# Kernel optimization log

Hardware: AMD Instinct MI355X
Metric: run time of the kernel (lower is better)

The kernel has to match this reference:

```python
import jax, jax.numpy as jnp
import numpy as np


def setup_inputs() -> dict:
    key = jax.random.key(0)
    k1, k2 = jax.random.split(key)
    x = jax.random.normal(k1, (131072, 256), dtype=jnp.float32)
    centroids = jax.random.normal(k2, (2048, 256), dtype=jnp.float32)
    return {"x": x, "centroids": centroids}


def reference(x, centroids):
    """One k-means step: L2 nearest-centroid assignment + scatter-mean update.

    x:         (n, d) sample vectors
    centroids: (K, d) current centroids
    returns:   (K, d) new centroids
    """
    K = centroids.shape[0]
    # Squared L2 distance argmin; ||x||^2 term is constant per row, drop it.
    # scores[n, K] = ||c_k||^2 - 2 * x_n . c_k
    c_sq = jnp.sum(centroids * centroids, axis=-1)          # (K,)
    scores = c_sq[None, :] - 2.0 * jnp.einsum("nd,kd->nk", x, centroids)
    assigns = jnp.argmin(scores, axis=-1)                    # (n,) int
    # Segment mean update; keep old centroid for empty clusters.
    sums = jax.ops.segment_sum(x, assigns, num_segments=K)   # (K, d)
    counts = jax.ops.segment_sum(jnp.ones((x.shape[0],), x.dtype), assigns,
                                 num_segments=K)             # (K,)
    nonempty = counts > 0
    means = sums / jnp.maximum(counts, 1.0)[:, None]
    new_centroids = jnp.where(nonempty[:, None], means, centroids)
    return new_centroids
```

## Files before the change

### kernel.cpp

```cpp
#include <hip/hip_runtime.h>

typedef unsigned short u16;
typedef unsigned int u32;
typedef unsigned long long u64;
typedef __attribute__((ext_vector_type(4)))  int  i32x4;
typedef __attribute__((ext_vector_type(16))) int  i32x16;
typedef __attribute__((ext_vector_type(16))) char i8x16;

#define NPTS 131072
#define DIM  256
#define KC   2048

constexpr float S1  = 0.0625f;
constexpr float S2  = S1 / 254.0f;
constexpr float S3  = S2 * S2 / S1;
constexpr float IS1 = 16.0f;
constexpr float IS2 = 4064.0f;
constexpr float IS3 = 1.0f / S3;
constexpr float W_A = S1 * S1;
constexpr float R2  = 1.0f / 254.0f;

__device__ inline void quant3(float v, char& q1, char& q2, char& q3) {
    float a = fminf(fmaxf(rintf(v * IS1), -127.f), 127.f);
    float r1 = fmaf(-a, S1, v);
    float b = rintf(r1 * IS2);
    float r2 = fmaf(-b, S2, r1);
    float c = rintf(r2 * IS3);
    q1 = (char)a; q2 = (char)b; q3 = (char)c;
}

#define GLD16(gsrc, ldst) \
    __builtin_amdgcn_global_load_lds( \
        (const __attribute__((address_space(1))) void*)(gsrc), \
        (__attribute__((address_space(3))) void*)(ldst), 16, 0, 0)

__global__ void cprep_kernel(const float* __restrict__ cen,
                             char* __restrict__ c_q,
                             int* __restrict__ c_sqi,
                             int* __restrict__ hist) {
    if (blockIdx.x < 8) hist[blockIdx.x * 256 + threadIdx.x] = 0;
    const int lane = threadIdx.x & 63;
    const int wv   = threadIdx.x >> 6;
    const int n    = blockIdx.x * 4 + wv;
    float4 v = ((const float4*)(cen + (size_t)n * DIM))[lane];
    float ss = v.x * v.x + v.y * v.y + v.z * v.z + v.w * v.w;
    float fv[4] = {v.x, v.y, v.z, v.w};
    char q1[4], q2[4], q3[4];
#pragma unroll
    for (int j = 0; j < 4; ++j) quant3(fv[j], q1[j], q2[j], q3[j]);
    const int g = n >> 5, r32 = n & 31;
    const int s = lane >> 2;
    const size_t base = ((size_t)((g * 16 + s) * 32 + r32)) * 16 + (lane & 3) * 4;
    u32 p1 = (u32)(unsigned char)q1[0] | ((u32)(unsigned char)q1[1] << 8) |
             ((u32)(unsigned char)q1[2] << 16) | ((u32)(unsigned char)q1[3] << 24);
    u32 p2 = (u32)(unsigned char)q2[0] | ((u32)(unsigned char)q2[1] << 8) |
             ((u32)(unsigned char)q2[2] << 16) | ((u32)(unsigned char)q2[3] << 24);
    u32 p3 = (u32)(unsigned char)q3[0] | ((u32)(unsigned char)q3[1] << 8) |
             ((u32)(unsigned char)q3[2] << 16) | ((u32)(unsigned char)q3[3] << 24);
    *(u32*)(c_q + base) = p1;
    *(u32*)(c_q + (size_t)KC * DIM + base) = p2;
    *(u32*)(c_q + (size_t)2 * KC * DIM + base) = p3;
#pragma unroll
    for (int off = 32; off > 0; off >>= 1) ss += __shfl_xor(ss, off);
    if (lane == 0) c_sqi[n] = (int)rintf(ss * (0.5f * 254.0f / W_A));
}

__global__ __launch_bounds__(256, 3) void assign_kernel(
    const float* __restrict__ x, const char* __restrict__ c_q,
    const int* __restrict__ c_sqi, int* __restrict__ assigns,
    int* __restrict__ hist) {
    __shared__ char lds_c[3 * 12288 + 8192];

    const int tid  = threadIdx.x;
    const int lane = tid & 63;
    const int wv   = tid >> 6;
    const int l31  = lane & 31;
    const int kh   = lane >> 5;

    const char* cl1 = c_q;
    const char* cl2 = c_q + (size_t)KC * DIM;
    const char* cl3 = c_q + (size_t)2 * KC * DIM;

    GLD16((const char*)c_sqi + tid * 16,         lds_c + 36864 + tid * 16);
    GLD16((const char*)c_sqi + (tid + 256) * 16, lds_c + 36864 + (tid + 256) * 16);
    GLD16(cl1 + tid * 16,        lds_c + tid * 16);
    GLD16(cl2 + tid * 16,        lds_c + 4096 + tid * 16);
    GLD16(cl3 + tid * 16,        lds_c + 8192 + tid * 16);
    GLD16(cl1 + 4096 + tid * 16, lds_c + 12288 + tid * 16);
    GLD16(cl2 + 4096 + tid * 16, lds_c + 12288 + 4096 + tid * 16);
    GLD16(cl3 + 4096 + tid * 16, lds_c + 12288 + 8192 + tid * 16);

    const int m = blockIdx.x * 128 + wv * 32 + l31;
    const float4* xr = (const float4*)(x + (size_t)m * DIM);
    i8x16 xq1[8], xq2[8], xq3[8];
#pragma unroll
    for (int kt = 0; kt < 8; ++kt) {
        float tmp[16];
#pragma unroll
        for (int j = 0; j < 4; ++j) {
            float4 f = xr[kt * 8 + kh * 4 + j];
            tmp[j * 4 + 0] = f.x; tmp[j * 4 + 1] = f.y;
            tmp[j * 4 + 2] = f.z; tmp[j * 4 + 3] = f.w;
        }
        i8x16 v1, v2, v3;
#pragma unroll
        for (int j = 0; j < 16; ++j) {
            char a, b, c;
            quant3(tmp[j], a, b, c);
            v1[j] = a; v2[j] = b; v3[j] = c;
        }
        xq1[kt] = v1; xq2[kt] = v2; xq3[kt] = v3;
    }

    __syncthreads();

    float best = 3.4e38f;
    int bidx = 0;
    int b3 = 0;

    const int* csqL = (const int*)(lds_c + 36864);

    for (int t = 0; t < 64; ++t) {
        i32x16 accA = {}, accB = {}, accC = {};
#pragma unroll
        for (int h2 = 0; h2 < 2; ++h2) {
            if (t == 63 && h2 == 1) {
                asm volatile("s_waitcnt vmcnt(0)" ::: "memory");
            } else {
                asm volatile("s_waitcnt vmcnt(3)" ::: "memory");
            }
            __builtin_amdgcn_s_barrier();
            __builtin_amdgcn_sched_barrier(0);
            if (2 * t + h2 + 2 < 128) {
                int pn = b3 + 2; if (pn >= 3) pn -= 3;
                char* d = lds_c + pn * 12288;
                const size_t so = (size_t)(2 * t + h2 + 2) * 4096;
                GLD16(cl1 + so + tid * 16, d + tid * 16);
                GLD16(cl2 + so + tid * 16, d + 4096 + tid * 16);
                GLD16(cl3 + so + tid * 16, d + 8192 + tid * 16);
            }
            const char* cb = lds_c + b3 * 12288;
            __builtin_amdgcn_s_setprio(1);
#pragma unroll
            for (int kt2 = 0; kt2 < 4; ++kt2) {
                const int off = kt2 * 1024 + kh * 512 + l31 * 16;
                i32x4 c1 = __builtin_bit_cast(i32x4, *(const i8x16*)(cb + off));
                i32x4 c2 = __builtin_bit_cast(i32x4, *(const i8x16*)(cb + 4096 + off));
                i32x4 c3 = __builtin_bit_cast(i32x4, *(const i8x16*)(cb + 8192 + off));
                i32x4 x1 = __builtin_bit_cast(i32x4, xq1[h2 * 4 + kt2]);
                i32x4 x2 = __builtin_bit_cast(i32x4, xq2[h2 * 4 + kt2]);
                i32x4 x3 = __builtin_bit_cast(i32x4, xq3[h2 * 4 + kt2]);
                accA = __builtin_amdgcn_mfma_i32_32x32x32_i8(c1, x1, accA, 0, 0, 0);
                accB = __builtin_amdgcn_mfma_i32_32x32x32_i8(c1, x2, accB, 0, 0, 0);
                accC = __builtin_amdgcn_mfma_i32_32x32x32_i8(c2, x2, accC, 0, 0, 0);
                accB = __builtin_amdgcn_mfma_i32_32x32x32_i8(c2, x1, accB, 0, 0, 0);
                accC = __builtin_amdgcn_mfma_i32_32x32x32_i8(c1, x3, accC, 0, 0, 0);
                accC = __builtin_amdgcn_mfma_i32_32x32x32_i8(c3, x1, accC, 0, 0, 0);
            }
            __builtin_amdgcn_s_setprio(0);
            b3 += 1; if (b3 == 3) b3 = 0;
        }

#pragma unroll
        for (int bq = 0; bq < 4; ++bq) {
            int4 cs = *(const int4*)(csqL + (t * 8 + 2 * bq + kh) * 4);
            const int n0 = t * 32 + 8 * bq + 4 * kh;
            int csa[4] = {cs.x, cs.y, cs.z, cs.w};
#pragma unroll
            for (int r = 0; r < 4; ++r) {
                const int idx = bq * 4 + r;
                int D  = __mul24(accA[idx], 254) + accB[idx];
                int Vi = csa[r] - D;
                float v = fmaf((float)accC[idx], -R2, (float)Vi);
                if (v < best) { best = v; bidx = n0 + r; }
            }
        }
    }

    float oval = __shfl_xor(best, 32);
    int   oidx = __shfl_xor(bidx, 32);
    if (oval < best || (oval == best && oidx < bidx)) { best = oval; bidx = oidx; }
    if (lane < 32) {
        assigns[m] = bidx;
        atomicAdd(&hist[bidx], 1);
    }
}

__global__ void scan_kernel(const int* __restrict__ hist,
                            int* __restrict__ base_,
                            int* __restrict__ cursor) {
    __shared__ int tmp[256];
    const int tid = threadIdx.x;
    int v[8], s = 0;
#pragma unroll
    for (int j = 0; j < 8; ++j) { v[j] = hist[tid * 8 + j]; s += v[j]; }
    tmp[tid] = s;
    __syncthreads();
    for (int off = 1; off < 256; off <<= 1) {
        int t = (tid >= off) ? tmp[tid - off] : 0;
        __syncthreads();
        tmp[tid] += t;
        __syncthreads();
    }
    int ex = tmp[tid] - s;
#pragma unroll
    for (int j = 0; j < 8; ++j) {
        base_[tid * 8 + j] = ex;
        cursor[tid * 8 + j] = ex;
        ex += v[j];
    }
}

__global__ void reorder_kernel(const int* __restrict__ assigns,
                               int* __restrict__ cursor,
                               int* __restrict__ order) {
    const int p = blockIdx.x * 256 + threadIdx.x;
    const int a = assigns[p];
    int pos = atomicAdd(&cursor[a], 1);
    order[pos] = p;
}

__global__ void reduce_kernel(const float* __restrict__ x,
                              const int* __restrict__ order,
                              const int* __restrict__ assigns,
                              float* __restrict__ sums) {
    const int tid = threadIdx.x;
    const int r0 = blockIdx.x * 256;
    float acc = 0.f;
    int cur = assigns[order[r0]];
    for (int r = 0; r < 256; r += 4) {
        int p0 = order[r0 + r + 0], p1 = order[r0 + r + 1];
        int p2 = order[r0 + r + 2], p3 = order[r0 + r + 3];
        float v0 = x[(size_t)p0 * DIM + tid];
        float v1 = x[(size_t)p1 * DIM + tid];
        float v2 = x[(size_t)p2 * DIM + tid];
        float v3 = x[(size_t)p3 * DIM + tid];
        int a0 = assigns[p0], a1 = assigns[p1], a2 = assigns[p2], a3 = assigns[p3];
        if (a0 != cur) { unsafeAtomicAdd(&sums[(size_t)cur * DIM + tid], acc); acc = 0.f; cur = a0; }
        acc += v0;
        if (a1 != cur) { unsafeAtomicAdd(&sums[(size_t)cur * DIM + tid], acc); acc = 0.f; cur = a1; }
        acc += v1;
        if (a2 != cur) { unsafeAtomicAdd(&sums[(size_t)cur * DIM + tid], acc); acc = 0.f; cur = a2; }
        acc += v2;
        if (a3 != cur) { unsafeAtomicAdd(&sums[(size_t)cur * DIM + tid], acc); acc = 0.f; cur = a3; }
        acc += v3;
    }
    unsafeAtomicAdd(&sums[(size_t)cur * DIM + tid], acc);
}

__global__ void finalize_kernel(const float* __restrict__ sums,
                                const int* __restrict__ hist,
                                const float* __restrict__ cen,
                                float* __restrict__ out) {
    const int id = blockIdx.x * 256 + threadIdx.x;
    const int k = id >> 6;
    const int cnt = hist[k];
    float4 s = ((const float4*)sums)[id];
    float4 c = ((const float4*)cen)[id];
    float4 o;
    if (cnt > 0) {
        float r = 1.0f / (float)cnt;
        o.x = s.x * r; o.y = s.y * r; o.z = s.z * r; o.w = s.w * r;
    } else {
        o = c;
    }
    ((float4*)out)[id] = o;
}

extern "C" void kernel_launch(void* const* d_in, const int* in_sizes, int n_in,
                              void* d_out, int out_size, void* d_ws, size_t ws_size,
                              hipStream_t stream) {
    (void)in_sizes; (void)n_in; (void)out_size; (void)ws_size;
    const float* x   = (const float*)d_in[0];
    const float* cen = (const float*)d_in[1];
    float* out = (float*)d_out;

    char* ws = (char*)d_ws;
    size_t off = 0;
    char* c_q = (char*)(ws + off);           off += (size_t)3 * KC * DIM;
    int* c_sqi = (int*)(ws + off);           off += (size_t)KC * 4;
    int* assigns = (int*)(ws + off);         off += (size_t)NPTS * 4;
    int* hist = (int*)(ws + off);            off += (size_t)KC * 4;
    int* base_ = (int*)(ws + off);           off += (size_t)KC * 4;
    int* cursor = (int*)(ws + off);          off += (size_t)KC * 4;
    int* order = (int*)(ws + off);           off += (size_t)NPTS * 4;
    float* sums = (float*)(ws + off);        off += (size_t)KC * DIM * 4;

    hipMemsetAsync(sums, 0, (size_t)KC * DIM * sizeof(float), stream);
    cprep_kernel<<<KC / 4, 256, 0, stream>>>(cen, c_q, c_sqi, hist);
    assign_kernel<<<NPTS / 128, 256, 0, stream>>>(x, c_q, c_sqi, assigns, hist);
    scan_kernel<<<1, 256, 0, stream>>>(hist, base_, cursor);
    reorder_kernel<<<NPTS / 256, 256, 0, stream>>>(assigns, cursor, order);
    reduce_kernel<<<NPTS / 256, 256, 0, stream>>>(x, order, assigns, sums);
    finalize_kernel<<<KC * 64 / 256, 256, 0, stream>>>(sums, hist, cen, out);
}
```

Measured before the change: 615.3 us.

## Switch centroid staging to double buffering, split accumulator chain, fuse sums zeroing

The assign kernel's LDS staging goes from a triple-buffered ring with a vmcnt(3) lookahead to a double buffer that waits on vmcnt(0) before each barrier. This cuts LDS use from about 45 KB to about 33 KB per block, which could let more blocks share a CU. The accC dependency chain of three MFMAs is split into two accumulators (accC and accC2) that are summed at the end, which shortens the serial MFMA dependence. The separate hipMemsetAsync of sums is folded into cprep_kernel, dropping one launch; the cost is less prefetch lookahead, so load latency may be exposed more often.

```diff
diff --git a/kernel.cpp b/kernel.cpp
--- a/kernel.cpp
+++ b/kernel.cpp
@@ -37,8 +37,10 @@
 __global__ void cprep_kernel(const float* __restrict__ cen,
                              char* __restrict__ c_q,
                              int* __restrict__ c_sqi,
-                             int* __restrict__ hist) {
+                             int* __restrict__ hist,
+                             float* __restrict__ sums) {
     if (blockIdx.x < 8) hist[blockIdx.x * 256 + threadIdx.x] = 0;
+    ((float4*)sums)[blockIdx.x * 256 + threadIdx.x] = (float4){0.f, 0.f, 0.f, 0.f};
     const int lane = threadIdx.x & 63;
     const int wv   = threadIdx.x >> 6;
     const int n    = blockIdx.x * 4 + wv;
@@ -69,7 +71,7 @@
     const float* __restrict__ x, const char* __restrict__ c_q,
     const int* __restrict__ c_sqi, int* __restrict__ assigns,
     int* __restrict__ hist) {
-    __shared__ char lds_c[3 * 12288 + 8192];
+    __shared__ char lds_c[2 * 12288 + 8192];
 
     const int tid  = threadIdx.x;
     const int lane = tid & 63;
@@ -81,14 +83,11 @@
     const char* cl2 = c_q + (size_t)KC * DIM;
     const char* cl3 = c_q + (size_t)2 * KC * DIM;
 
-    GLD16((const char*)c_sqi + tid * 16,         lds_c + 36864 + tid * 16);
-    GLD16((const char*)c_sqi + (tid + 256) * 16, lds_c + 36864 + (tid + 256) * 16);
-    GLD16(cl1 + tid * 16,        lds_c + tid * 16);
-    GLD16(cl2 + tid * 16,        lds_c + 4096 + tid * 16);
-    GLD16(cl3 + tid * 16,        lds_c + 8192 + tid * 16);
-    GLD16(cl1 + 4096 + tid * 16, lds_c + 12288 + tid * 16);
-    GLD16(cl2 + 4096 + tid * 16, lds_c + 12288 + 4096 + tid * 16);
-    GLD16(cl3 + 4096 + tid * 16, lds_c + 12288 + 8192 + tid * 16);
+    GLD16((const char*)c_sqi + tid * 16,         lds_c + 24576 + tid * 16);
+    GLD16((const char*)c_sqi + (tid + 256) * 16, lds_c + 24576 + (tid + 256) * 16);
+    GLD16(cl1 + tid * 16, lds_c + tid * 16);
+    GLD16(cl2 + tid * 16, lds_c + 4096 + tid * 16);
+    GLD16(cl3 + tid * 16, lds_c + 8192 + tid * 16);
 
     const int m = blockIdx.x * 128 + wv * 32 + l31;
     const float4* xr = (const float4*)(x + (size_t)m * DIM);
@@ -112,34 +111,27 @@
         xq1[kt] = v1; xq2[kt] = v2; xq3[kt] = v3;
     }
 
-    __syncthreads();
-
     float best = 3.4e38f;
     int bidx = 0;
-    int b3 = 0;
-
-    const int* csqL = (const int*)(lds_c + 36864);
+
+    const int* csqL = (const int*)(lds_c + 24576);
 
     for (int t = 0; t < 64; ++t) {
-        i32x16 accA = {}, accB = {}, accC = {};
+        i32x16 accA = {}, accB = {}, accC = {}, accC2 = {};
 #pragma unroll
         for (int h2 = 0; h2 < 2; ++h2) {
-            if (t == 63 && h2 == 1) {
-                asm volatile("s_waitcnt vmcnt(0)" ::: "memory");
-            } else {
-                asm volatile("s_waitcnt vmcnt(3)" ::: "memory");
-            }
+            const int u = 2 * t + h2;
+            asm volatile("s_waitcnt vmcnt(0)" ::: "memory");
             __builtin_amdgcn_s_barrier();
             __builtin_amdgcn_sched_barrier(0);
-            if (2 * t + h2 + 2 < 128) {
-                int pn = b3 + 2; if (pn >= 3) pn -= 3;
-                char* d = lds_c + pn * 12288;
-                const size_t so = (size_t)(2 * t + h2 + 2) * 4096;
+            if (u + 1 < 128) {
+                char* d = lds_c + ((u + 1) & 1) * 12288;
+                const size_t so = (size_t)(u + 1) * 4096;
                 GLD16(cl1 + so + tid * 16, d + tid * 16);
                 GLD16(cl2 + so + tid * 16, d + 4096 + tid * 16);
                 GLD16(cl3 + so + tid * 16, d + 8192 + tid * 16);
             }
-            const char* cb = lds_c + b3 * 12288;
+            const char* cb = lds_c + (u & 1) * 12288;
             __builtin_amdgcn_s_setprio(1);
 #pragma unroll
             for (int kt2 = 0; kt2 < 4; ++kt2) {
@@ -150,15 +142,14 @@
                 i32x4 x1 = __builtin_bit_cast(i32x4, xq1[h2 * 4 + kt2]);
                 i32x4 x2 = __builtin_bit_cast(i32x4, xq2[h2 * 4 + kt2]);
                 i32x4 x3 = __builtin_bit_cast(i32x4, xq3[h2 * 4 + kt2]);
-                accA = __builtin_amdgcn_mfma_i32_32x32x32_i8(c1, x1, accA, 0, 0, 0);
-                accB = __builtin_amdgcn_mfma_i32_32x32x32_i8(c1, x2, accB, 0, 0, 0);
-                accC = __builtin_amdgcn_mfma_i32_32x32x32_i8(c2, x2, accC, 0, 0, 0);
-                accB = __builtin_amdgcn_mfma_i32_32x32x32_i8(c2, x1, accB, 0, 0, 0);
-                accC = __builtin_amdgcn_mfma_i32_32x32x32_i8(c1, x3, accC, 0, 0, 0);
-                accC = __builtin_amdgcn_mfma_i32_32x32x32_i8(c3, x1, accC, 0, 0, 0);
+                accA  = __builtin_amdgcn_mfma_i32_32x32x32_i8(c1, x1, accA,  0, 0, 0);
+                accB  = __builtin_amdgcn_mfma_i32_32x32x32_i8(c1, x2, accB,  0, 0, 0);
+                accC2 = __builtin_amdgcn_mfma_i32_32x32x32_i8(c1, x3, accC2, 0, 0, 0);
+                accC  = __builtin_amdgcn_mfma_i32_32x32x32_i8(c2, x2, accC,  0, 0, 0);
+                accB  = __builtin_amdgcn_mfma_i32_32x32x32_i8(c2, x1, accB,  0, 0, 0);
+                accC2 = __builtin_amdgcn_mfma_i32_32x32x32_i8(c3, x1, accC2, 0, 0, 0);
             }
             __builtin_amdgcn_s_setprio(0);
-            b3 += 1; if (b3 == 3) b3 = 0;
         }
 
 #pragma unroll
@@ -170,8 +161,9 @@
             for (int r = 0; r < 4; ++r) {
                 const int idx = bq * 4 + r;
                 int D  = __mul24(accA[idx], 254) + accB[idx];
+                int Ci = accC[idx] + accC2[idx];
                 int Vi = csa[r] - D;
-                float v = fmaf((float)accC[idx], -R2, (float)Vi);
+                float v = fmaf((float)Ci, -R2, (float)Vi);
                 if (v < best) { best = v; bidx = n0 + r; }
             }
         }
@@ -286,8 +278,7 @@
     int* order = (int*)(ws + off);           off += (size_t)NPTS * 4;
     float* sums = (float*)(ws + off);        off += (size_t)KC * DIM * 4;
 
-    hipMemsetAsync(sums, 0, (size_t)KC * DIM * sizeof(float), stream);
-    cprep_kernel<<<KC / 4, 256, 0, stream>>>(cen, c_q, c_sqi, hist);
+    cprep_kernel<<<KC / 4, 256, 0, stream>>>(cen, c_q, c_sqi, hist, sums);
     assign_kernel<<<NPTS / 128, 256, 0, stream>>>(x, c_q, c_sqi, assigns, hist);
     scan_kernel<<<1, 256, 0, stream>>>(hist, base_, cursor);
     reorder_kernel<<<NPTS / 256, 256, 0, stream>>>(assigns, cursor, order);
```

Result: slower. 678.8 us (+10.3%).

## Process two 32-row point tiles per wave and fold sums memset into cprep

Applied to the files above, without the earlier changes.

Each wave now quantizes and scores 64 points instead of 32, reusing every centroid fragment loaded from LDS across two sets of MFMA accumulators. This halves the LDS reads and centroid staging per point, and the block count drops by half. In exchange, register pressure roughly doubles, so launch bounds go from 3 to 2 blocks per CU. The separate memset of the sums buffer is removed, and cprep_kernel now zeroes it, which saves a launch. The __syncthreads after the x quantization was also dropped, but the loop's first waitcnt and barrier still cover the initial LDS loads.

```diff
diff --git a/kernel.cpp b/kernel.cpp
--- a/kernel.cpp
+++ b/kernel.cpp
@@ -29,6 +29,25 @@
     q1 = (char)a; q2 = (char)b; q3 = (char)c;
 }
 
+__device__ inline void quant_frag(const float4* __restrict__ xr, int kt, int kh,
+                                  i8x16& o1, i8x16& o2, i8x16& o3) {
+    float tmp[16];
+#pragma unroll
+    for (int j = 0; j < 4; ++j) {
+        float4 f = xr[kt * 8 + kh * 4 + j];
+        tmp[j * 4 + 0] = f.x; tmp[j * 4 + 1] = f.y;
+        tmp[j * 4 + 2] = f.z; tmp[j * 4 + 3] = f.w;
+    }
+    i8x16 v1, v2, v3;
+#pragma unroll
+    for (int j = 0; j < 16; ++j) {
+        char a, b, c;
+        quant3(tmp[j], a, b, c);
+        v1[j] = a; v2[j] = b; v3[j] = c;
+    }
+    o1 = v1; o2 = v2; o3 = v3;
+}
+
 #define GLD16(gsrc, ldst) \
     __builtin_amdgcn_global_load_lds( \
         (const __attribute__((address_space(1))) void*)(gsrc), \
@@ -37,8 +56,10 @@
 __global__ void cprep_kernel(const float* __restrict__ cen,
                              char* __restrict__ c_q,
                              int* __restrict__ c_sqi,
-                             int* __restrict__ hist) {
+                             int* __restrict__ hist,
+                             float* __restrict__ sums) {
     if (blockIdx.x < 8) hist[blockIdx.x * 256 + threadIdx.x] = 0;
+    ((float4*)sums)[blockIdx.x * 256 + threadIdx.x] = (float4){0.f, 0.f, 0.f, 0.f};
     const int lane = threadIdx.x & 63;
     const int wv   = threadIdx.x >> 6;
     const int n    = blockIdx.x * 4 + wv;
@@ -65,7 +86,7 @@
     if (lane == 0) c_sqi[n] = (int)rintf(ss * (0.5f * 254.0f / W_A));
 }
 
-__global__ __launch_bounds__(256, 3) void assign_kernel(
+__global__ __launch_bounds__(256, 2) void assign_kernel(
     const float* __restrict__ x, const char* __restrict__ c_q,
     const int* __restrict__ c_sqi, int* __restrict__ assigns,
     int* __restrict__ hist) {
@@ -90,38 +111,27 @@
     GLD16(cl2 + 4096 + tid * 16, lds_c + 12288 + 4096 + tid * 16);
     GLD16(cl3 + 4096 + tid * 16, lds_c + 12288 + 8192 + tid * 16);
 
-    const int m = blockIdx.x * 128 + wv * 32 + l31;
-    const float4* xr = (const float4*)(x + (size_t)m * DIM);
-    i8x16 xq1[8], xq2[8], xq3[8];
+    const int mbase = blockIdx.x * 256 + wv * 64;
+    const int mA = mbase + l31;
+    const int mB = mA + 32;
+    const float4* xrA = (const float4*)(x + (size_t)mA * DIM);
+    const float4* xrB = (const float4*)(x + (size_t)mB * DIM);
+    i8x16 xa1[8], xa2[8], xa3[8], xb1[8], xb2[8], xb3[8];
 #pragma unroll
     for (int kt = 0; kt < 8; ++kt) {
-        float tmp[16];
-#pragma unroll
-        for (int j = 0; j < 4; ++j) {
-            float4 f = xr[kt * 8 + kh * 4 + j];
-            tmp[j * 4 + 0] = f.x; tmp[j * 4 + 1] = f.y;
-            tmp[j * 4 + 2] = f.z; tmp[j * 4 + 3] = f.w;
-        }
-        i8x16 v1, v2, v3;
-#pragma unroll
-        for (int j = 0; j < 16; ++j) {
-            char a, b, c;
-            quant3(tmp[j], a, b, c);
-            v1[j] = a; v2[j] = b; v3[j] = c;
-        }
-        xq1[kt] = v1; xq2[kt] = v2; xq3[kt] = v3;
-    }
-
-    __syncthreads();
-
-    float best = 3.4e38f;
-    int bidx = 0;
+        quant_frag(xrA, kt, kh, xa1[kt], xa2[kt], xa3[kt]);
+        quant_frag(xrB, kt, kh, xb1[kt], xb2[kt], xb3[kt]);
+    }
+
+    float bestA = 3.4e38f, bestB = 3.4e38f;
+    int bixA = 0, bixB = 0;
     int b3 = 0;
 
     const int* csqL = (const int*)(lds_c + 36864);
 
     for (int t = 0; t < 64; ++t) {
-        i32x16 accA = {}, accB = {}, accC = {};
+        i32x16 accAa = {}, accBa = {}, accCa = {};
+        i32x16 accAb = {}, accBb = {}, accCb = {};
 #pragma unroll
         for (int h2 = 0; h2 < 2; ++h2) {
             if (t == 63 && h2 == 1) {
@@ -147,15 +157,25 @@
                 i32x4 c1 = __builtin_bit_cast(i32x4, *(const i8x16*)(cb + off));
                 i32x4 c2 = __builtin_bit_cast(i32x4, *(const i8x16*)(cb + 4096 + off));
                 i32x4 c3 = __builtin_bit_cast(i32x4, *(const i8x16*)(cb + 8192 + off));
-                i32x4 x1 = __builtin_bit_cast(i32x4, xq1[h2 * 4 + kt2]);
-                i32x4 x2 = __builtin_bit_cast(i32x4, xq2[h2 * 4 + kt2]);
-                i32x4 x3 = __builtin_bit_cast(i32x4, xq3[h2 * 4 + kt2]);
-                accA = __builtin_amdgcn_mfma_i32_32x32x32_i8(c1, x1, accA, 0, 0, 0);
-                accB = __builtin_amdgcn_mfma_i32_32x32x32_i8(c1, x2, accB, 0, 0, 0);
-                accC = __builtin_amdgcn_mfma_i32_32x32x32_i8(c2, x2, accC, 0, 0, 0);
-                accB = __builtin_amdgcn_mfma_i32_32x32x32_i8(c2, x1, accB, 0, 0, 0);
-                accC = __builtin_amdgcn_mfma_i32_32x32x32_i8(c1, x3, accC, 0, 0, 0);
-                accC = __builtin_amdgcn_mfma_i32_32x32x32_i8(c3, x1, accC, 0, 0, 0);
+                const int kq = h2 * 4 + kt2;
+                i32x4 a1 = __builtin_bit_cast(i32x4, xa1[kq]);
+                i32x4 a2 = __builtin_bit_cast(i32x4, xa2[kq]);
+                i32x4 a3 = __builtin_bit_cast(i32x4, xa3[kq]);
+                i32x4 b1 = __builtin_bit_cast(i32x4, xb1[kq]);
+                i32x4 b2 = __builtin_bit_cast(i32x4, xb2[kq]);
+                i32x4 b3v = __builtin_bit_cast(i32x4, xb3[kq]);
+                accAa = __builtin_amdgcn_mfma_i32_32x32x32_i8(c1, a1, accAa, 0, 0, 0);
+                accAb = __builtin_amdgcn_mfma_i32_32x32x32_i8(c1, b1, accAb, 0, 0, 0);
+                accBa = __builtin_amdgcn_mfma_i32_32x32x32_i8(c1, a2, accBa, 0, 0, 0);
+                accBb = __builtin_amdgcn_mfma_i32_32x32x32_i8(c1, b2, accBb, 0, 0, 0);
+                accCa = __builtin_amdgcn_mfma_i32_32x32x32_i8(c2, a2, accCa, 0, 0, 0);
+                accCb = __builtin_amdgcn_mfma_i32_32x32x32_i8(c2, b2, accCb, 0, 0, 0);
+                accBa = __builtin_amdgcn_mfma_i32_32x32x32_i8(c2, a1, accBa, 0, 0, 0);
+                accBb = __builtin_amdgcn_mfma_i32_32x32x32_i8(c2, b1, accBb, 0, 0, 0);
+                accCa = __builtin_amdgcn_mfma_i32_32x32x32_i8(c1, a3, accCa, 0, 0, 0);
+                accCb = __builtin_amdgcn_mfma_i32_32x32x32_i8(c1, b3v, accCb, 0, 0, 0);
+                accCa = __builtin_amdgcn_mfma_i32_32x32x32_i8(c3, a1, accCa, 0, 0, 0);
+                accCb = __builtin_amdgcn_mfma_i32_32x32x32_i8(c3, b1, accCb, 0, 0, 0);
             }
             __builtin_amdgcn_s_setprio(0);
             b3 += 1; if (b3 == 3) b3 = 0;
@@ -169,21 +189,25 @@
 #pragma unroll
             for (int r = 0; r < 4; ++r) {
                 const int idx = bq * 4 + r;
-                int D  = __mul24(accA[idx], 254) + accB[idx];
-                int Vi = csa[r] - D;
-                float v = fmaf((float)accC[idx], -R2, (float)Vi);
-                if (v < best) { best = v; bidx = n0 + r; }
+                int Da = __mul24(accAa[idx], 254) + accBa[idx];
+                float va = fmaf((float)accCa[idx], -R2, (float)(csa[r] - Da));
+                if (va < bestA) { bestA = va; bixA = n0 + r; }
+                int Db = __mul24(accAb[idx], 254) + accBb[idx];
+                float vb = fmaf((float)accCb[idx], -R2, (float)(csa[r] - Db));
+                if (vb < bestB) { bestB = vb; bixB = n0 + r; }
             }
         }
     }
 
-    float oval = __shfl_xor(best, 32);
-    int   oidx = __shfl_xor(bidx, 32);
-    if (oval < best || (oval == best && oidx < bidx)) { best = oval; bidx = oidx; }
-    if (lane < 32) {
-        assigns[m] = bidx;
-        atomicAdd(&hist[bidx], 1);
-    }
+    float ovA = __shfl_xor(bestA, 32);
+    int   oiA = __shfl_xor(bixA, 32);
+    if (ovA < bestA || (ovA == bestA && oiA < bixA)) { bestA = ovA; bixA = oiA; }
+    float ovB = __shfl_xor(bestB, 32);
+    int   oiB = __shfl_xor(bixB, 32);
+    if (ovB < bestB || (ovB == bestB && oiB < bixB)) { bestB = ovB; bixB = oiB; }
+    const int myIdx = (lane < 32) ? bixA : bixB;
+    assigns[mbase + lane] = myIdx;
+    atomicAdd(&hist[myIdx], 1);
 }
 
 __global__ void scan_kernel(const int* __restrict__ hist,
@@ -286,9 +310,8 @@
     int* order = (int*)(ws + off);           off += (size_t)NPTS * 4;
     float* sums = (float*)(ws + off);        off += (size_t)KC * DIM * 4;
 
-    hipMemsetAsync(sums, 0, (size_t)KC * DIM * sizeof(float), stream);
-    cprep_kernel<<<KC / 4, 256, 0, stream>>>(cen, c_q, c_sqi, hist);
-    assign_kernel<<<NPTS / 128, 256, 0, stream>>>(x, c_q, c_sqi, assigns, hist);
+    cprep_kernel<<<KC / 4, 256, 0, stream>>>(cen, c_q, c_sqi, hist, sums);
+    assign_kernel<<<NPTS / 256, 256, 0, stream>>>(x, c_q, c_sqi, assigns, hist);
     scan_kernel<<<1, 256, 0, stream>>>(hist, base_, cursor);
     reorder_kernel<<<NPTS / 256, 256, 0, stream>>>(assigns, cursor, order);
     reduce_kernel<<<NPTS / 256, 256, 0, stream>>>(x, order, assigns, sums);
```

New measurement: 749.2 us. 1.22x slower.

## Split centroid range into halves with persistent work-queue assign kernel and atomicMin merge

Applied to the files above, without the earlier changes.

The assign kernel becomes persistent with 768 blocks that pull work items from an atomic counter. Each item covers 128 points against half of the centroids, and partial argmins are merged through a 64-bit atomicMin on a packed (score, index) key. A new resolve kernel then writes the assignments and the histogram. Zeroing of sums moves from a memset into cprep, and the C accumulator is split in two to shorten the MFMA dependency chain. The aim is better load balance and fewer wave-quantization tail effects, at the cost of quantizing x twice per point, extra atomics and one extra kernel launch.

```diff
diff --git a/kernel.cpp b/kernel.cpp
--- a/kernel.cpp
+++ b/kernel.cpp
@@ -10,6 +10,7 @@
 #define NPTS 131072
 #define DIM  256
 #define KC   2048
+#define NITEMS 2048
 
 constexpr float S1  = 0.0625f;
 constexpr float S2  = S1 / 254.0f;
@@ -29,6 +30,25 @@
     q1 = (char)a; q2 = (char)b; q3 = (char)c;
 }
 
+__device__ inline void quant_frag(const float4* __restrict__ xr, int kt, int kh,
+                                  i8x16& o1, i8x16& o2, i8x16& o3) {
+    float tmp[16];
+#pragma unroll
+    for (int j = 0; j < 4; ++j) {
+        float4 f = xr[kt * 8 + kh * 4 + j];
+        tmp[j * 4 + 0] = f.x; tmp[j * 4 + 1] = f.y;
+        tmp[j * 4 + 2] = f.z; tmp[j * 4 + 3] = f.w;
+    }
+    i8x16 v1, v2, v3;
+#pragma unroll
+    for (int j = 0; j < 16; ++j) {
+        char a, b, c;
+        quant3(tmp[j], a, b, c);
+        v1[j] = a; v2[j] = b; v3[j] = c;
+    }
+    o1 = v1; o2 = v2; o3 = v3;
+}
+
 #define GLD16(gsrc, ldst) \
     __builtin_amdgcn_global_load_lds( \
         (const __attribute__((address_space(1))) void*)(gsrc), \
@@ -37,8 +57,14 @@
 __global__ void cprep_kernel(const float* __restrict__ cen,
                              char* __restrict__ c_q,
                              int* __restrict__ c_sqi,
-                             int* __restrict__ hist) {
+                             int* __restrict__ hist,
+                             float* __restrict__ sums,
+                             u64* __restrict__ best_key,
+                             int* __restrict__ work) {
     if (blockIdx.x < 8) hist[blockIdx.x * 256 + threadIdx.x] = 0;
+    if (blockIdx.x == 8 && threadIdx.x == 0) *work = 0;
+    ((float4*)sums)[blockIdx.x * 256 + threadIdx.x] = (float4){0.f, 0.f, 0.f, 0.f};
+    best_key[blockIdx.x * 256 + threadIdx.x] = ~0ull;
     const int lane = threadIdx.x & 63;
     const int wv   = threadIdx.x >> 6;
     const int n    = blockIdx.x * 4 + wv;
@@ -67,9 +93,10 @@
 
 __global__ __launch_bounds__(256, 3) void assign_kernel(
     const float* __restrict__ x, const char* __restrict__ c_q,
-    const int* __restrict__ c_sqi, int* __restrict__ assigns,
-    int* __restrict__ hist) {
+    const int* __restrict__ c_sqi, u64* __restrict__ best_key,
+    int* __restrict__ work) {
     __shared__ char lds_c[3 * 12288 + 8192];
+    __shared__ int item_s;
 
     const int tid  = threadIdx.x;
     const int lane = tid & 63;
@@ -77,113 +104,119 @@
     const int l31  = lane & 31;
     const int kh   = lane >> 5;
 
-    const char* cl1 = c_q;
-    const char* cl2 = c_q + (size_t)KC * DIM;
-    const char* cl3 = c_q + (size_t)2 * KC * DIM;
-
     GLD16((const char*)c_sqi + tid * 16,         lds_c + 36864 + tid * 16);
     GLD16((const char*)c_sqi + (tid + 256) * 16, lds_c + 36864 + (tid + 256) * 16);
-    GLD16(cl1 + tid * 16,        lds_c + tid * 16);
-    GLD16(cl2 + tid * 16,        lds_c + 4096 + tid * 16);
-    GLD16(cl3 + tid * 16,        lds_c + 8192 + tid * 16);
-    GLD16(cl1 + 4096 + tid * 16, lds_c + 12288 + tid * 16);
-    GLD16(cl2 + 4096 + tid * 16, lds_c + 12288 + 4096 + tid * 16);
-    GLD16(cl3 + 4096 + tid * 16, lds_c + 12288 + 8192 + tid * 16);
-
-    const int m = blockIdx.x * 128 + wv * 32 + l31;
-    const float4* xr = (const float4*)(x + (size_t)m * DIM);
-    i8x16 xq1[8], xq2[8], xq3[8];
-#pragma unroll
-    for (int kt = 0; kt < 8; ++kt) {
-        float tmp[16];
-#pragma unroll
-        for (int j = 0; j < 4; ++j) {
-            float4 f = xr[kt * 8 + kh * 4 + j];
-            tmp[j * 4 + 0] = f.x; tmp[j * 4 + 1] = f.y;
-            tmp[j * 4 + 2] = f.z; tmp[j * 4 + 3] = f.w;
-        }
-        i8x16 v1, v2, v3;
-#pragma unroll
-        for (int j = 0; j < 16; ++j) {
-            char a, b, c;
-            quant3(tmp[j], a, b, c);
-            v1[j] = a; v2[j] = b; v3[j] = c;
-        }
-        xq1[kt] = v1; xq2[kt] = v2; xq3[kt] = v3;
-    }
-
-    __syncthreads();
-
-    float best = 3.4e38f;
-    int bidx = 0;
-    int b3 = 0;
-
     const int* csqL = (const int*)(lds_c + 36864);
 
-    for (int t = 0; t < 64; ++t) {
-        i32x16 accA = {}, accB = {}, accC = {};
-#pragma unroll
-        for (int h2 = 0; h2 < 2; ++h2) {
-            if (t == 63 && h2 == 1) {
-                asm volatile("s_waitcnt vmcnt(0)" ::: "memory");
-            } else {
-                asm volatile("s_waitcnt vmcnt(3)" ::: "memory");
+    for (;;) {
+        if (tid == 0) item_s = atomicAdd(work, 1);
+        __syncthreads();
+        const int it = item_s;
+        if (it >= NITEMS) break;
+        const int pc = it >> 1;
+        const int h  = it & 1;
+
+        const char* cl1 = c_q + (size_t)h * 262144;
+        const char* cl2 = c_q + (size_t)KC * DIM + (size_t)h * 262144;
+        const char* cl3 = c_q + (size_t)2 * KC * DIM + (size_t)h * 262144;
+
+        GLD16(cl1 + tid * 16,        lds_c + tid * 16);
+        GLD16(cl2 + tid * 16,        lds_c + 4096 + tid * 16);
+        GLD16(cl3 + tid * 16,        lds_c + 8192 + tid * 16);
+        GLD16(cl1 + 4096 + tid * 16, lds_c + 12288 + tid * 16);
+        GLD16(cl2 + 4096 + tid * 16, lds_c + 12288 + 4096 + tid * 16);
+        GLD16(cl3 + 4096 + tid * 16, lds_c + 12288 + 8192 + tid * 16);
+
+        const int m = pc * 128 + wv * 32 + l31;
+        const float4* xr = (const float4*)(x + (size_t)m * DIM);
+        i8x16 xq1[8], xq2[8], xq3[8];
+#pragma unroll
+        for (int kt = 0; kt < 8; ++kt)
+            quant_frag(xr, kt, kh, xq1[kt], xq2[kt], xq3[kt]);
+
+        float best = 3.4e38f;
+        int bidx = 0;
+        int b3 = 0;
+
+        for (int t = 0; t < 32; ++t) {
+            i32x16 accA = {}, accB = {}, accC = {}, accC2 = {};
+#pragma unroll
+            for (int h2 = 0; h2 < 2; ++h2) {
+                const int u = 2 * t + h2;
+                if (u == 63) {
+                    asm volatile("s_waitcnt vmcnt(0)" ::: "memory");
+                } else {
+                    asm volatile("s_waitcnt vmcnt(3)" ::: "memory");
+                }
+                __builtin_amdgcn_s_barrier();
+                __builtin_amdgcn_sched_barrier(0);
+                if (u + 2 < 64) {
+                    int pn = b3 + 2; if (pn >= 3) pn -= 3;
+                    char* d = lds_c + pn * 12288;
+                    const size_t so = (size_t)(u + 2) * 4096;
+                    GLD16(cl1 + so + tid * 16, d + tid * 16);
+                    GLD16(cl2 + so + tid * 16, d + 4096 + tid * 16);
+                    GLD16(cl3 + so + tid * 16, d + 8192 + tid * 16);
+                }
+                const char* cb = lds_c + b3 * 12288;
+                __builtin_amdgcn_s_setprio(1);
+#pragma unroll
+                for (int kt2 = 0; kt2 < 4; ++kt2) {
+                    const int off = kt2 * 1024 + kh * 512 + l31 * 16;
+                    i32x4 c1 = __builtin_bit_cast(i32x4, *(const i8x16*)(cb + off));
+                    i32x4 c2 = __builtin_bit_cast(i32x4, *(const i8x16*)(cb + 4096 + off));
+                    i32x4 c3 = __builtin_bit_cast(i32x4, *(const i8x16*)(cb + 8192 + off));
+                    i32x4 x1 = __builtin_bit_cast(i32x4, xq1[h2 * 4 + kt2]);
+                    i32x4 x2 = __builtin_bit_cast(i32x4, xq2[h2 * 4 + kt2]);
+                    i32x4 x3 = __builtin_bit_cast(i32x4, xq3[h2 * 4 + kt2]);
+                    accA  = __builtin_amdgcn_mfma_i32_32x32x32_i8(c1, x1, accA,  0, 0, 0);
+                    accB  = __builtin_amdgcn_mfma_i32_32x32x32_i8(c1, x2, accB,  0, 0, 0);
+                    accC2 = __builtin_amdgcn_mfma_i32_32x32x32_i8(c1, x3, accC2, 0, 0, 0);
+                    accC  = __builtin_amdgcn_mfma_i32_32x32x32_i8(c2, x2, accC,  0, 0, 0);
+                    accB  = __builtin_amdgcn_mfma_i32_32x32x32_i8(c2, x1, accB,  0, 0, 0);
+                    accC2 = __builtin_amdgcn_mfma_i32_32x32x32_i8(c3, x1, accC2, 0, 0, 0);
+                }
+                __builtin_amdgcn_s_setprio(0);
+                b3 += 1; if (b3 == 3) b3 = 0;
             }
-            __builtin_amdgcn_s_barrier();
-            __builtin_amdgcn_sched_barrier(0);
-            if (2 * t + h2 + 2 < 128) {
-                int pn = b3 + 2; if (pn >= 3) pn -= 3;
-                char* d = lds_c + pn * 12288;
-                const size_t so = (size_t)(2 * t + h2 + 2) * 4096;
-                GLD16(cl1 + so + tid * 16, d + tid * 16);
-                GLD16(cl2 + so + tid * 16, d + 4096 + tid * 16);
-                GLD16(cl3 + so + tid * 16, d + 8192 + tid * 16);
-            }
-            const char* cb = lds_c + b3 * 12288;
-            __builtin_amdgcn_s_setprio(1);
-#pragma unroll
-            for (int kt2 = 0; kt2 < 4; ++kt2) {
-                const int off = kt2 * 1024 + kh * 512 + l31 * 16;
-                i32x4 c1 = __builtin_bit_cast(i32x4, *(const i8x16*)(cb + off));
-                i32x4 c2 = __builtin_bit_cast(i32x4, *(const i8x16*)(cb + 4096 + off));
-                i32x4 c3 = __builtin_bit_cast(i32x4, *(const i8x16*)(cb + 8192 + off));
-                i32x4 x1 = __builtin_bit_cast(i32x4, xq1[h2 * 4 + kt2]);
-                i32x4 x2 = __builtin_bit_cast(i32x4, xq2[h2 * 4 + kt2]);
-                i32x4 x3 = __builtin_bit_cast(i32x4, xq3[h2 * 4 + kt2]);
-                accA = __builtin_amdgcn_mfma_i32_32x32x32_i8(c1, x1, accA, 0, 0, 0);
-                accB = __builtin_amdgcn_mfma_i32_32x32x32_i8(c1, x2, accB, 0, 0, 0);
-                accC = __builtin_amdgcn_mfma_i32_32x32x32_i8(c2, x2, accC, 0, 0, 0);
-                accB = __builtin_amdgcn_mfma_i32_32x32x32_i8(c2, x1, accB, 0, 0, 0);
-                accC = __builtin_amdgcn_mfma_i32_32x32x32_i8(c1, x3, accC, 0, 0, 0);
-                accC = __builtin_amdgcn_mfma_i32_32x32x32_i8(c3, x1, accC, 0, 0, 0);
-            }
-            __builtin_amdgcn_s_setprio(0);
-            b3 += 1; if (b3 == 3) b3 = 0;
-        }
-
-#pragma unroll
-        for (int bq = 0; bq < 4; ++bq) {
-            int4 cs = *(const int4*)(csqL + (t * 8 + 2 * bq + kh) * 4);
-            const int n0 = t * 32 + 8 * bq + 4 * kh;
-            int csa[4] = {cs.x, cs.y, cs.z, cs.w};
-#pragma unroll
-            for (int r = 0; r < 4; ++r) {
-                const int idx = bq * 4 + r;
-                int D  = __mul24(accA[idx], 254) + accB[idx];
-                int Vi = csa[r] - D;
-                float v = fmaf((float)accC[idx], -R2, (float)Vi);
-                if (v < best) { best = v; bidx = n0 + r; }
+
+            const int nt = h * 32 + t;
+#pragma unroll
+            for (int bq = 0; bq < 4; ++bq) {
+                int4 cs = *(const int4*)(csqL + (nt * 8 + 2 * bq + kh) * 4);
+                const int n0 = nt * 32 + 8 * bq + 4 * kh;
+                int csa[4] = {cs.x, cs.y, cs.z, cs.w};
+#pragma unroll
+                for (int r = 0; r < 4; ++r) {
+                    const int idx = bq * 4 + r;
+                    int D  = __mul24(accA[idx], 254) + accB[idx];
+                    int Ci = accC[idx] + accC2[idx];
+                    int Vi = csa[r] - D;
+                    float v = fmaf((float)Ci, -R2, (float)Vi);
+                    if (v < best) { best = v; bidx = n0 + r; }
+                }
             }
         }
-    }
-
-    float oval = __shfl_xor(best, 32);
-    int   oidx = __shfl_xor(bidx, 32);
-    if (oval < best || (oval == best && oidx < bidx)) { best = oval; bidx = oidx; }
-    if (lane < 32) {
-        assigns[m] = bidx;
-        atomicAdd(&hist[bidx], 1);
-    }
+
+        float oval = __shfl_xor(best, 32);
+        int   oidx = __shfl_xor(bidx, 32);
+        if (oval < best || (oval == best && oidx < bidx)) { best = oval; bidx = oidx; }
+        if (lane < 32) {
+            u32 sb = __float_as_uint(best);
+            sb = (sb & 0x80000000u) ? ~sb : (sb | 0x80000000u);
+            u64 key = ((u64)sb << 32) | (u32)bidx;
+            atomicMin(&best_key[m], key);
+        }
+    }
+}
+
+__global__ void resolve_kernel(const u64* __restrict__ best_key,
+                               int* __restrict__ assigns,
+                               int* __restrict__ hist) {
+    const int m = blockIdx.x * 256 + threadIdx.x;
+    const int idx = (int)(u32)(best_key[m] & 0xffffffffu);
+    assigns[m] = idx;
+    atomicAdd(&hist[idx], 1);
 }
 
 __global__ void scan_kernel(const int* __restrict__ hist,
@@ -285,10 +318,13 @@
     int* cursor = (int*)(ws + off);          off += (size_t)KC * 4;
     int* order = (int*)(ws + off);           off += (size_t)NPTS * 4;
     float* sums = (float*)(ws + off);        off += (size_t)KC * DIM * 4;
-
-    hipMemsetAsync(sums, 0, (size_t)KC * DIM * sizeof(float), stream);
-    cprep_kernel<<<KC / 4, 256, 0, stream>>>(cen, c_q, c_sqi, hist);
-    assign_kernel<<<NPTS / 128, 256, 0, stream>>>(x, c_q, c_sqi, assigns, hist);
+    u64* best_key = (u64*)(ws + off);        off += (size_t)NPTS * 8;
+    int* work = (int*)(ws + off);            off += 4096;
+
+    cprep_kernel<<<KC / 4, 256, 0, stream>>>(cen, c_q, c_sqi, hist, sums,
+                                             best_key, work);
+    assign_kernel<<<768, 256, 0, stream>>>(x, c_q, c_sqi, best_key, work);
+    resolve_kernel<<<NPTS / 256, 256, 0, stream>>>(best_key, assigns, hist);
     scan_kernel<<<1, 256, 0, stream>>>(hist, base_, cursor);
     reorder_kernel<<<NPTS / 256, 256, 0, stream>>>(assigns, cursor, order);
     reduce_kernel<<<NPTS / 256, 256, 0, stream>>>(x, order, assigns, sums);
```

Measured after the change: 779.6 us. 26.7% more time.
